# Kernel tuning notes

Hardware: AMD Instinct MI355X
Metric: run time of the kernel (lower is better)

The kernel has to match this reference:

```python
import jax, jax.numpy as jnp
import numpy as np

U, P, D, H, E = 512, 1024, 128, 256, 98304
N = U + P


def setup_inputs() -> dict:
    key = jax.random.key(0)
    ks = jax.random.split(key, 16)
    def nrm(k, shape, scale=0.05):
        return jax.random.normal(k, shape, jnp.float32) * scale
    z = lambda *s: jnp.zeros(s, jnp.float32)
    return {
        "user_ids": jnp.arange(U),
        "paper_ids": jnp.arange(P),
        "edge_index": jax.random.randint(ks[0], (2, E), 0, N),
        "user_paper_interactions": jax.random.uniform(ks[1], (U, P), jnp.float32),
        "user_emb": nrm(ks[2], (U, D), 1.0),   # nn.Embedding tables
        "paper_emb": nrm(ks[3], (P, D), 1.0),
        "W0": nrm(ks[4], (D, H)), "b0": z(H),   # GCNConv weights (stored [in,out])
        "W1": nrm(ks[5], (H, H)), "b1": z(H),
        "W2": nrm(ks[6], (H, H)), "b2": z(H),
        "Wu": nrm(ks[7], (H, D)), "bu": z(D),   # user_output Linear
        "Wp": nrm(ks[8], (H, D)), "bp": z(D),   # paper_output Linear
        "Wq1": nrm(ks[9], (2 * D, H)), "bq1": z(H),  # predictor Linear 1
        "Wq2": nrm(ks[10], (H, 1)), "bq2": z(1),      # predictor Linear 2
    }


def gcn_conv(x, src, dst, W, b):
    """PyG GCNConv: add self-loops, symmetric D^-1/2 (A+I) D^-1/2 normalization."""
    n = x.shape[0]
    loop = jnp.arange(n)
    s = jnp.concatenate([src, loop])
    d = jnp.concatenate([dst, loop])
    deg = jax.ops.segment_sum(jnp.ones(d.shape, x.dtype), d, num_segments=n)
    dis = jnp.where(deg > 0, jax.lax.rsqrt(jnp.maximum(deg, 1.0)), 0.0)
    norm = dis[s] * dis[d]                      # [E+n]
    h = x @ W                                   # [n, H]
    out = jax.ops.segment_sum(h[s] * norm[:, None], d, num_segments=n)
    return out + b


def reference(user_ids, paper_ids, edge_index, user_paper_interactions,
              user_emb, paper_emb, W0, b0, W1, b1, W2, b2,
              Wu, bu, Wp, bp, Wq1, bq1, Wq2, bq2):
    # embedding lookups + node feature matrix [U+P, D]
    x = jnp.concatenate([user_emb[user_ids], paper_emb[paper_ids]], axis=0)
    src, dst = edge_index[0], edge_index[1]
    for W, b in ((W0, b0), (W1, b1), (W2, b2)):
        x = jax.nn.relu(gcn_conv(x, src, dst, W, b))  # dropout is identity in eval
    nu = user_ids.shape[0]
    np_ = paper_ids.shape[0]
    user_final = x[:nu] @ Wu + bu               # [U, D]
    paper_final = x[nu:] @ Wp + bp              # [P, D]
    # broadcast outer-product concat -> [U, P, 2D]
    combined = jnp.concatenate([
        jnp.broadcast_to(user_final[:, None, :], (nu, np_, user_final.shape[-1])),
        jnp.broadcast_to(paper_final[None, :, :], (nu, np_, paper_final.shape[-1])),
    ], axis=-1)
    h = jax.nn.relu(combined @ Wq1 + bq1)       # [U, P, H]
    pred = jax.nn.sigmoid(h @ Wq2 + bq2)[..., 0]  # [U, P]
    return pred
```

## Files before the change

### kernel.cpp

```cpp
#include <hip/hip_runtime.h>
#include <math.h>

constexpr int Uc = 512;
constexpr int Pc = 1024;
constexpr int Dc = 128;
constexpr int Hc = 256;
constexpr int Ec = 98304;
constexpr int Nc = 1536;
constexpr int CAP = 192;

template <int K>
__device__ __forceinline__ void gemm_core16(const float* __restrict__ xr,
                                            const float* __restrict__ wc, int M,
                                            float& acc0, float& acc1) {
#pragma unroll 4
    for (int k = 0; k < K; k += 4) {
        float4 a = *(const float4*)(xr + k);
        float2 b0 = *(const float2*)(wc + (size_t)k * M);
        float2 b1 = *(const float2*)(wc + (size_t)(k + 1) * M);
        float2 b2 = *(const float2*)(wc + (size_t)(k + 2) * M);
        float2 b3 = *(const float2*)(wc + (size_t)(k + 3) * M);
        acc0 += a.x * b0.x; acc1 += a.x * b0.y;
        acc0 += a.y * b1.x; acc1 += a.y * b1.y;
        acc0 += a.z * b2.x; acc1 += a.z * b2.y;
        acc0 += a.w * b3.x; acc1 += a.w * b3.y;
    }
}

__global__ void k_front(const int* __restrict__ e_src, const int* __restrict__ e_dst,
                        int* __restrict__ cnt, int* __restrict__ colF,
                        const float* __restrict__ Wu, const float* __restrict__ Wp,
                        const float* __restrict__ Wq1, const float* __restrict__ bu,
                        const float* __restrict__ bp, const float* __restrict__ bq1,
                        float* __restrict__ Wup, float* __restrict__ Wpp,
                        float* __restrict__ bvu, float* __restrict__ bvp) {
    int t = threadIdx.x, b = blockIdx.x;
    if (b < 384) {
        int e = b * 256 + t;
        int d = e_dst[e];
        int pos = atomicAdd(&cnt[d], 1);
        if (pos < CAP) colF[d * CAP + pos] = e_src[e];
    } else if (b < 640) {
        int id = b - 384;
        int z = id >> 7, tile = id & 127;
        int tx = t & 15, ty = t >> 4;
        const float* X = z ? Wp : Wu;
        const float* W = Wq1 + (z ? (size_t)Dc * Hc : 0);
        float* Y = z ? Wpp : Wup;
        int row = (tile >> 3) * 16 + ty, col = (tile & 7) * 32 + tx * 2;
        float a0 = 0.f, a1 = 0.f;
        gemm_core16<Dc>(X + (size_t)row * Dc, W + col, Hc, a0, a1);
        *(float2*)&Y[(size_t)row * Hc + col] = make_float2(a0, a1);
    } else if (b == 640) {
        float s = bq1[t];
#pragma unroll 8
        for (int d = 0; d < Dc; d++) s += bu[d] * Wq1[d * Hc + t];
        bvu[t] = s;
    } else {
        float s = 0.f;
#pragma unroll 8
        for (int d = 0; d < Dc; d++) s += bp[d] * Wq1[(Dc + d) * Hc + t];
        bvp[t] = s;
    }
}

__global__ void k_l0(const int* __restrict__ uid, const int* __restrict__ pid,
                     const float* __restrict__ ue, const float* __restrict__ pe,
                     const float* __restrict__ W0, const float* __restrict__ b0,
                     const int* __restrict__ cnt, const int* __restrict__ colF,
                     float* __restrict__ out) {
    __shared__ const float* sptr[2][CAP];
    __shared__ float snrm[2][CAP];
    __shared__ __align__(16) float agg[2][Dc];
    int t = threadIdx.x, b = blockIdx.x;
    int i0 = b * 2, i1 = b * 2 + 1;
    int c0 = cnt[i0], c1 = cnt[i1];
    int deg0 = min(c0, CAP), deg1 = min(c1, CAP);
    float di0 = rsqrtf((float)(c0 + 1)), di1 = rsqrtf((float)(c1 + 1));
    if (t < deg0) {
        int s = colF[i0 * CAP + t];
        sptr[0][t] = (s < Uc) ? ue + (size_t)uid[s] * Dc : pe + (size_t)pid[s - Uc] * Dc;
        snrm[0][t] = rsqrtf((float)(cnt[s] + 1));
    }
    if (t < deg1) {
        int s = colF[i1 * CAP + t];
        sptr[1][t] = (s < Uc) ? ue + (size_t)uid[s] * Dc : pe + (size_t)pid[s - Uc] * Dc;
        snrm[1][t] = rsqrtf((float)(cnt[s] + 1));
    }
    __syncthreads();
    {
        int r = t >> 7, f = t & 127;
        int i = b * 2 + r;
        float di = r ? di1 : di0;
        int dg = r ? deg1 : deg0;
        const float* xi = (i < Uc) ? ue + (size_t)uid[i] * Dc : pe + (size_t)pid[i - Uc] * Dc;
        float acc = di * xi[f];
        int j = 0;
        for (; j + 4 <= dg; j += 4) {
            float v0 = snrm[r][j]     * sptr[r][j][f];
            float v1 = snrm[r][j + 1] * sptr[r][j + 1][f];
            float v2 = snrm[r][j + 2] * sptr[r][j + 2][f];
            float v3 = snrm[r][j + 3] * sptr[r][j + 3][f];
            acc += (v0 + v1) + (v2 + v3);
        }
        for (; j < dg; j++) acc += snrm[r][j] * sptr[r][j][f];
        agg[r][f] = di * acc;
    }
    __syncthreads();
    float acc0 = 0.f, acc1 = 0.f;
#pragma unroll 4
    for (int k = 0; k < Dc; k += 4) {
        float4 a0 = *(const float4*)&agg[0][k];
        float4 a1 = *(const float4*)&agg[1][k];
        float w0 = W0[(size_t)(k + 0) * Hc + t];
        float w1 = W0[(size_t)(k + 1) * Hc + t];
        float w2 = W0[(size_t)(k + 2) * Hc + t];
        float w3 = W0[(size_t)(k + 3) * Hc + t];
        acc0 += a0.x * w0 + a0.y * w1 + a0.z * w2 + a0.w * w3;
        acc1 += a1.x * w0 + a1.y * w1 + a1.z * w2 + a1.w * w3;
    }
    float bb = b0[t];
    out[(size_t)i0 * Hc + t] = fmaxf(acc0 + bb, 0.f);
    out[(size_t)i1 * Hc + t] = fmaxf(acc1 + bb, 0.f);
}

__global__ void k_lh(const float* __restrict__ X, const float* __restrict__ W,
                     const float* __restrict__ bias, const int* __restrict__ cnt,
                     const int* __restrict__ colF, float* __restrict__ out) {
    __shared__ int sidx[2][CAP];
    __shared__ float snrm[2][CAP];
    __shared__ __align__(16) float agg[2][Hc];
    int t = threadIdx.x, b = blockIdx.x;
    int i0 = b * 2, i1 = b * 2 + 1;
    int c0 = cnt[i0], c1 = cnt[i1];
    int deg0 = min(c0, CAP), deg1 = min(c1, CAP);
    float di0 = rsqrtf((float)(c0 + 1)), di1 = rsqrtf((float)(c1 + 1));
    if (t < deg0) {
        int s = colF[i0 * CAP + t];
        sidx[0][t] = s * Hc;
        snrm[0][t] = rsqrtf((float)(cnt[s] + 1));
    }
    if (t < deg1) {
        int s = colF[i1 * CAP + t];
        sidx[1][t] = s * Hc;
        snrm[1][t] = rsqrtf((float)(cnt[s] + 1));
    }
    __syncthreads();
    {
        float acc = di0 * X[(size_t)i0 * Hc + t];
        int j = 0;
        for (; j + 4 <= deg0; j += 4) {
            float v0 = snrm[0][j]     * X[sidx[0][j] + t];
            float v1 = snrm[0][j + 1] * X[sidx[0][j + 1] + t];
            float v2 = snrm[0][j + 2] * X[sidx[0][j + 2] + t];
            float v3 = snrm[0][j + 3] * X[sidx[0][j + 3] + t];
            acc += (v0 + v1) + (v2 + v3);
        }
        for (; j < deg0; j++) acc += snrm[0][j] * X[sidx[0][j] + t];
        agg[0][t] = di0 * acc;
    }
    {
        float acc = di1 * X[(size_t)i1 * Hc + t];
        int j = 0;
        for (; j + 4 <= deg1; j += 4) {
            float v0 = snrm[1][j]     * X[sidx[1][j] + t];
            float v1 = snrm[1][j + 1] * X[sidx[1][j + 1] + t];
            float v2 = snrm[1][j + 2] * X[sidx[1][j + 2] + t];
            float v3 = snrm[1][j + 3] * X[sidx[1][j + 3] + t];
            acc += (v0 + v1) + (v2 + v3);
        }
        for (; j < deg1; j++) acc += snrm[1][j] * X[sidx[1][j] + t];
        agg[1][t] = di1 * acc;
    }
    __syncthreads();
    float acc0 = 0.f, acc1 = 0.f;
#pragma unroll 4
    for (int k = 0; k < Hc; k += 4) {
        float4 a0 = *(const float4*)&agg[0][k];
        float4 a1 = *(const float4*)&agg[1][k];
        float w0 = W[(size_t)(k + 0) * Hc + t];
        float w1 = W[(size_t)(k + 1) * Hc + t];
        float w2 = W[(size_t)(k + 2) * Hc + t];
        float w3 = W[(size_t)(k + 3) * Hc + t];
        acc0 += a0.x * w0 + a0.y * w1 + a0.z * w2 + a0.w * w3;
        acc1 += a1.x * w0 + a1.y * w1 + a1.z * w2 + a1.w * w3;
    }
    float bb = bias[t];
    out[(size_t)i0 * Hc + t] = fmaxf(acc0 + bb, 0.f);
    out[(size_t)i1 * Hc + t] = fmaxf(acc1 + bb, 0.f);
}

__global__ void k_gemm_t(const float* __restrict__ xA, const float* __restrict__ Wup,
                         const float* __restrict__ Wpp, const float* __restrict__ bvu,
                         const float* __restrict__ bvp, float* __restrict__ AuT,
                         float* __restrict__ ApT) {
    int t = threadIdx.x, tx = t & 15, ty = t >> 4;
    int it = blockIdx.x;
    const float* X; const float* W; const float* bias; float* YT; int ldy; int id;
    if (it < 256) { X = xA;                   W = Wup; bias = bvu; YT = AuT; ldy = Uc; id = it; }
    else          { X = xA + (size_t)Uc * Hc; W = Wpp; bias = bvp; YT = ApT; ldy = Pc; id = it - 256; }
    int rloc = (id >> 3) * 16 + ty, col = (id & 7) * 32 + tx * 2;
    float a0 = 0.f, a1 = 0.f;
    gemm_core16<Hc>(X + (size_t)rloc * Hc, W + col, Hc, a0, a1);
    YT[(size_t)col * ldy + rloc]       = a0 + bias[col];
    YT[(size_t)(col + 1) * ldy + rloc] = a1 + bias[col + 1];
}

__global__ void k_pred(const float* __restrict__ AuT, const float* __restrict__ ApT,
                       const float* __restrict__ Wq2, const float* __restrict__ bq2,
                       float* __restrict__ out) {
    __shared__ float auS[Hc * 16];
    int t = threadIdx.x;
    int ub = blockIdx.x * 16, pb = blockIdx.y * 64;
#pragma unroll
    for (int i = t; i < Hc * 16; i += 256) {
        int k = i >> 4, u = i & 15;
        auS[i] = AuT[(size_t)k * Uc + ub + u];
    }
    __syncthreads();
    int uu = t >> 5;
    int pp = t & 31;
    const float* app = ApT + pb + pp * 2;
    const float* aup = auS + uu * 2;
    float acc[2][2] = {};
#pragma unroll 4
    for (int k = 0; k < Hc; k += 4) {
        float4 wv = *(const float4*)&Wq2[k];
        float2 a[4], p2[4];
#pragma unroll
        for (int j = 0; j < 4; j++) a[j] = *(const float2*)(aup + (k + j) * 16);
#pragma unroll
        for (int j = 0; j < 4; j++) p2[j] = *(const float2*)(app + (size_t)(k + j) * Pc);
        const float* w = (const float*)&wv;
#pragma unroll
        for (int j = 0; j < 4; j++) {
            float a0 = a[j].x, a1 = a[j].y;
            float p0 = p2[j].x, p1 = p2[j].y;
            acc[0][0] += fmaxf(a0 + p0, 0.f) * w[j];
            acc[0][1] += fmaxf(a0 + p1, 0.f) * w[j];
            acc[1][0] += fmaxf(a1 + p0, 0.f) * w[j];
            acc[1][1] += fmaxf(a1 + p1, 0.f) * w[j];
        }
    }
    float bq = bq2[0];
#pragma unroll
    for (int r = 0; r < 2; r++) {
        int u = ub + uu * 2 + r;
        float2 o;
        o.x = 1.f / (1.f + __expf(-(acc[r][0] + bq)));
        o.y = 1.f / (1.f + __expf(-(acc[r][1] + bq)));
        *(float2*)&out[(size_t)u * Pc + pb + pp * 2] = o;
    }
}


extern "C" void kernel_launch(void* const* d_in, const int* in_sizes, int n_in,
                              void* d_out, int out_size, void* d_ws, size_t ws_size,
                              hipStream_t stream) {
    const int*   uid = (const int*)d_in[0];
    const int*   pid = (const int*)d_in[1];
    const int*   ei  = (const int*)d_in[2];
    const float* ue  = (const float*)d_in[4];
    const float* pe  = (const float*)d_in[5];
    const float* W0  = (const float*)d_in[6];  const float* b0 = (const float*)d_in[7];
    const float* W1  = (const float*)d_in[8];  const float* b1 = (const float*)d_in[9];
    const float* W2  = (const float*)d_in[10]; const float* b2 = (const float*)d_in[11];
    const float* Wu  = (const float*)d_in[12]; const float* bu = (const float*)d_in[13];
    const float* Wp  = (const float*)d_in[14]; const float* bp = (const float*)d_in[15];
    const float* Wq1 = (const float*)d_in[16]; const float* bq1 = (const float*)d_in[17];
    const float* Wq2 = (const float*)d_in[18]; const float* bq2 = (const float*)d_in[19];

    const int* e_src = ei;
    const int* e_dst = ei + Ec;

    char* w = (char*)d_ws;
    auto alloc = [&](size_t bytes) { char* p = w; w += (bytes + 255) & ~size_t(255); return p; };
    int*   cnt  = (int*)alloc(Nc * 4);
    int*   colF = (int*)alloc((size_t)Nc * CAP * 4);
    float* xA   = (float*)alloc((size_t)Nc * Hc * 4);
    float* xB   = (float*)alloc((size_t)Nc * Hc * 4);
    float* Wup  = (float*)alloc((size_t)Hc * Hc * 4);
    float* Wpp  = (float*)alloc((size_t)Hc * Hc * 4);
    float* bvu  = (float*)alloc(Hc * 4);
    float* bvp  = (float*)alloc(Hc * 4);
    float* AuT  = (float*)alloc((size_t)Hc * Uc * 4);
    float* ApT  = (float*)alloc((size_t)Hc * Pc * 4);
    float* pred = (float*)d_out;

    hipMemsetAsync(cnt, 0, Nc * 4, stream);
    k_front<<<642, 256, 0, stream>>>(e_src, e_dst, cnt, colF, Wu, Wp, Wq1,
                                     bu, bp, bq1, Wup, Wpp, bvu, bvp);
    k_l0<<<Nc / 2, 256, 0, stream>>>(uid, pid, ue, pe, W0, b0, cnt, colF, xA);
    k_lh<<<Nc / 2, 256, 0, stream>>>(xA, W1, b1, cnt, colF, xB);
    k_lh<<<Nc / 2, 256, 0, stream>>>(xB, W2, b2, cnt, colF, xA);
    k_gemm_t<<<768, 256, 0, stream>>>(xA, Wup, Wpp, bvu, bvp, AuT, ApT);
    k_pred<<<dim3(Uc / 16, Pc / 64), 256, 0, stream>>>(AuT, ApT, Wq2, bq2, pred);
}
```

Before: 232.9 us.

## Process four nodes per block and fuse final GCN layer with output projection

```diff
diff --git a/kernel.cpp b/kernel.cpp
--- a/kernel.cpp
+++ b/kernel.cpp
@@ -69,32 +69,34 @@
                      const float* __restrict__ W0, const float* __restrict__ b0,
                      const int* __restrict__ cnt, const int* __restrict__ colF,
                      float* __restrict__ out) {
-    __shared__ const float* sptr[2][CAP];
-    __shared__ float snrm[2][CAP];
-    __shared__ __align__(16) float agg[2][Dc];
+    __shared__ const float* sptr[4][CAP];
+    __shared__ float snrm[4][CAP];
+    __shared__ __align__(16) float agg[4][Dc];
     int t = threadIdx.x, b = blockIdx.x;
-    int i0 = b * 2, i1 = b * 2 + 1;
-    int c0 = cnt[i0], c1 = cnt[i1];
-    int deg0 = min(c0, CAP), deg1 = min(c1, CAP);
-    float di0 = rsqrtf((float)(c0 + 1)), di1 = rsqrtf((float)(c1 + 1));
-    if (t < deg0) {
-        int s = colF[i0 * CAP + t];
-        sptr[0][t] = (s < Uc) ? ue + (size_t)uid[s] * Dc : pe + (size_t)pid[s - Uc] * Dc;
-        snrm[0][t] = rsqrtf((float)(cnt[s] + 1));
-    }
-    if (t < deg1) {
-        int s = colF[i1 * CAP + t];
-        sptr[1][t] = (s < Uc) ? ue + (size_t)uid[s] * Dc : pe + (size_t)pid[s - Uc] * Dc;
-        snrm[1][t] = rsqrtf((float)(cnt[s] + 1));
-    }
-    __syncthreads();
-    {
-        int r = t >> 7, f = t & 127;
-        int i = b * 2 + r;
-        float di = r ? di1 : di0;
-        int dg = r ? deg1 : deg0;
-        const float* xi = (i < Uc) ? ue + (size_t)uid[i] * Dc : pe + (size_t)pid[i - Uc] * Dc;
-        float acc = di * xi[f];
+    int ibase = b * 4;
+    int c[4]; float di[4];
+#pragma unroll
+    for (int r = 0; r < 4; r++) {
+        c[r] = cnt[ibase + r];
+        di[r] = rsqrtf((float)(c[r] + 1));
+        int deg = min(c[r], CAP);
+        if (t < deg) {
+            int s = colF[(ibase + r) * CAP + t];
+            sptr[r][t] = (s < Uc) ? ue + (size_t)uid[s] * Dc
+                                  : pe + (size_t)pid[s - Uc] * Dc;
+            snrm[r][t] = rsqrtf((float)(cnt[s] + 1));
+        }
+    }
+    __syncthreads();
+    int r2 = t >> 7, f = t & 127;
+#pragma unroll
+    for (int rr = 0; rr < 4; rr += 2) {
+        int r = rr + r2;
+        int i = ibase + r;
+        int dg = min(c[r], CAP);
+        const float* xi = (i < Uc) ? ue + (size_t)uid[i] * Dc
+                                   : pe + (size_t)pid[i - Uc] * Dc;
+        float acc = di[r] * xi[f];
         int j = 0;
         for (; j + 4 <= dg; j += 4) {
             float v0 = snrm[r][j]     * sptr[r][j][f];
@@ -104,106 +106,183 @@
             acc += (v0 + v1) + (v2 + v3);
         }
         for (; j < dg; j++) acc += snrm[r][j] * sptr[r][j][f];
-        agg[r][f] = di * acc;
-    }
-    __syncthreads();
-    float acc0 = 0.f, acc1 = 0.f;
-#pragma unroll 4
+        agg[r][f] = di[r] * acc;
+    }
+    __syncthreads();
+    float a0 = 0.f, a1 = 0.f, a2 = 0.f, a3 = 0.f;
+#pragma unroll 2
     for (int k = 0; k < Dc; k += 4) {
-        float4 a0 = *(const float4*)&agg[0][k];
-        float4 a1 = *(const float4*)&agg[1][k];
+        float4 g0 = *(const float4*)&agg[0][k];
+        float4 g1 = *(const float4*)&agg[1][k];
+        float4 g2 = *(const float4*)&agg[2][k];
+        float4 g3 = *(const float4*)&agg[3][k];
         float w0 = W0[(size_t)(k + 0) * Hc + t];
         float w1 = W0[(size_t)(k + 1) * Hc + t];
         float w2 = W0[(size_t)(k + 2) * Hc + t];
         float w3 = W0[(size_t)(k + 3) * Hc + t];
-        acc0 += a0.x * w0 + a0.y * w1 + a0.z * w2 + a0.w * w3;
-        acc1 += a1.x * w0 + a1.y * w1 + a1.z * w2 + a1.w * w3;
+        a0 += g0.x * w0 + g0.y * w1 + g0.z * w2 + g0.w * w3;
+        a1 += g1.x * w0 + g1.y * w1 + g1.z * w2 + g1.w * w3;
+        a2 += g2.x * w0 + g2.y * w1 + g2.z * w2 + g2.w * w3;
+        a3 += g3.x * w0 + g3.y * w1 + g3.z * w2 + g3.w * w3;
     }
     float bb = b0[t];
-    out[(size_t)i0 * Hc + t] = fmaxf(acc0 + bb, 0.f);
-    out[(size_t)i1 * Hc + t] = fmaxf(acc1 + bb, 0.f);
+    out[(size_t)(ibase + 0) * Hc + t] = fmaxf(a0 + bb, 0.f);
+    out[(size_t)(ibase + 1) * Hc + t] = fmaxf(a1 + bb, 0.f);
+    out[(size_t)(ibase + 2) * Hc + t] = fmaxf(a2 + bb, 0.f);
+    out[(size_t)(ibase + 3) * Hc + t] = fmaxf(a3 + bb, 0.f);
 }
 
 __global__ void k_lh(const float* __restrict__ X, const float* __restrict__ W,
                      const float* __restrict__ bias, const int* __restrict__ cnt,
                      const int* __restrict__ colF, float* __restrict__ out) {
-    __shared__ int sidx[2][CAP];
-    __shared__ float snrm[2][CAP];
-    __shared__ __align__(16) float agg[2][Hc];
+    __shared__ int sidx[4][CAP];
+    __shared__ float snrm[4][CAP];
+    __shared__ __align__(16) float agg[4][Hc];
     int t = threadIdx.x, b = blockIdx.x;
-    int i0 = b * 2, i1 = b * 2 + 1;
-    int c0 = cnt[i0], c1 = cnt[i1];
-    int deg0 = min(c0, CAP), deg1 = min(c1, CAP);
-    float di0 = rsqrtf((float)(c0 + 1)), di1 = rsqrtf((float)(c1 + 1));
-    if (t < deg0) {
-        int s = colF[i0 * CAP + t];
-        sidx[0][t] = s * Hc;
-        snrm[0][t] = rsqrtf((float)(cnt[s] + 1));
-    }
-    if (t < deg1) {
-        int s = colF[i1 * CAP + t];
-        sidx[1][t] = s * Hc;
-        snrm[1][t] = rsqrtf((float)(cnt[s] + 1));
-    }
-    __syncthreads();
-    {
-        float acc = di0 * X[(size_t)i0 * Hc + t];
+    int ibase = b * 4;
+    int c[4]; float di[4];
+#pragma unroll
+    for (int r = 0; r < 4; r++) {
+        c[r] = cnt[ibase + r];
+        di[r] = rsqrtf((float)(c[r] + 1));
+        int deg = min(c[r], CAP);
+        if (t < deg) {
+            int s = colF[(ibase + r) * CAP + t];
+            sidx[r][t] = s * Hc;
+            snrm[r][t] = rsqrtf((float)(cnt[s] + 1));
+        }
+    }
+    __syncthreads();
+#pragma unroll
+    for (int r = 0; r < 4; r++) {
+        int dg = min(c[r], CAP);
+        float acc = di[r] * X[(size_t)(ibase + r) * Hc + t];
         int j = 0;
-        for (; j + 4 <= deg0; j += 4) {
-            float v0 = snrm[0][j]     * X[sidx[0][j] + t];
-            float v1 = snrm[0][j + 1] * X[sidx[0][j + 1] + t];
-            float v2 = snrm[0][j + 2] * X[sidx[0][j + 2] + t];
-            float v3 = snrm[0][j + 3] * X[sidx[0][j + 3] + t];
+        for (; j + 4 <= dg; j += 4) {
+            float v0 = snrm[r][j]     * X[sidx[r][j] + t];
+            float v1 = snrm[r][j + 1] * X[sidx[r][j + 1] + t];
+            float v2 = snrm[r][j + 2] * X[sidx[r][j + 2] + t];
+            float v3 = snrm[r][j + 3] * X[sidx[r][j + 3] + t];
             acc += (v0 + v1) + (v2 + v3);
         }
-        for (; j < deg0; j++) acc += snrm[0][j] * X[sidx[0][j] + t];
-        agg[0][t] = di0 * acc;
-    }
-    {
-        float acc = di1 * X[(size_t)i1 * Hc + t];
-        int j = 0;
-        for (; j + 4 <= deg1; j += 4) {
-            float v0 = snrm[1][j]     * X[sidx[1][j] + t];
-            float v1 = snrm[1][j + 1] * X[sidx[1][j + 1] + t];
-            float v2 = snrm[1][j + 2] * X[sidx[1][j + 2] + t];
-            float v3 = snrm[1][j + 3] * X[sidx[1][j + 3] + t];
-            acc += (v0 + v1) + (v2 + v3);
-        }
-        for (; j < deg1; j++) acc += snrm[1][j] * X[sidx[1][j] + t];
-        agg[1][t] = di1 * acc;
-    }
-    __syncthreads();
-    float acc0 = 0.f, acc1 = 0.f;
-#pragma unroll 4
+        for (; j < dg; j++) acc += snrm[r][j] * X[sidx[r][j] + t];
+        agg[r][t] = di[r] * acc;
+    }
+    __syncthreads();
+    float a0 = 0.f, a1 = 0.f, a2 = 0.f, a3 = 0.f;
+#pragma unroll 2
     for (int k = 0; k < Hc; k += 4) {
-        float4 a0 = *(const float4*)&agg[0][k];
-        float4 a1 = *(const float4*)&agg[1][k];
+        float4 g0 = *(const float4*)&agg[0][k];
+        float4 g1 = *(const float4*)&agg[1][k];
+        float4 g2 = *(const float4*)&agg[2][k];
+        float4 g3 = *(const float4*)&agg[3][k];
         float w0 = W[(size_t)(k + 0) * Hc + t];
         float w1 = W[(size_t)(k + 1) * Hc + t];
         float w2 = W[(size_t)(k + 2) * Hc + t];
         float w3 = W[(size_t)(k + 3) * Hc + t];
-        acc0 += a0.x * w0 + a0.y * w1 + a0.z * w2 + a0.w * w3;
-        acc1 += a1.x * w0 + a1.y * w1 + a1.z * w2 + a1.w * w3;
+        a0 += g0.x * w0 + g0.y * w1 + g0.z * w2 + g0.w * w3;
+        a1 += g1.x * w0 + g1.y * w1 + g1.z * w2 + g1.w * w3;
+        a2 += g2.x * w0 + g2.y * w1 + g2.z * w2 + g2.w * w3;
+        a3 += g3.x * w0 + g3.y * w1 + g3.z * w2 + g3.w * w3;
     }
     float bb = bias[t];
-    out[(size_t)i0 * Hc + t] = fmaxf(acc0 + bb, 0.f);
-    out[(size_t)i1 * Hc + t] = fmaxf(acc1 + bb, 0.f);
-}
-
-__global__ void k_gemm_t(const float* __restrict__ xA, const float* __restrict__ Wup,
-                         const float* __restrict__ Wpp, const float* __restrict__ bvu,
-                         const float* __restrict__ bvp, float* __restrict__ AuT,
-                         float* __restrict__ ApT) {
-    int t = threadIdx.x, tx = t & 15, ty = t >> 4;
-    int it = blockIdx.x;
-    const float* X; const float* W; const float* bias; float* YT; int ldy; int id;
-    if (it < 256) { X = xA;                   W = Wup; bias = bvu; YT = AuT; ldy = Uc; id = it; }
-    else          { X = xA + (size_t)Uc * Hc; W = Wpp; bias = bvp; YT = ApT; ldy = Pc; id = it - 256; }
-    int rloc = (id >> 3) * 16 + ty, col = (id & 7) * 32 + tx * 2;
-    float a0 = 0.f, a1 = 0.f;
-    gemm_core16<Hc>(X + (size_t)rloc * Hc, W + col, Hc, a0, a1);
-    YT[(size_t)col * ldy + rloc]       = a0 + bias[col];
-    YT[(size_t)(col + 1) * ldy + rloc] = a1 + bias[col + 1];
+    out[(size_t)(ibase + 0) * Hc + t] = fmaxf(a0 + bb, 0.f);
+    out[(size_t)(ibase + 1) * Hc + t] = fmaxf(a1 + bb, 0.f);
+    out[(size_t)(ibase + 2) * Hc + t] = fmaxf(a2 + bb, 0.f);
+    out[(size_t)(ibase + 3) * Hc + t] = fmaxf(a3 + bb, 0.f);
+}
+
+__global__ void k_lht(const float* __restrict__ X, const float* __restrict__ W2,
+                      const float* __restrict__ b2, const int* __restrict__ cnt,
+                      const int* __restrict__ colF,
+                      const float* __restrict__ Wup, const float* __restrict__ Wpp,
+                      const float* __restrict__ bvu, const float* __restrict__ bvp,
+                      float* __restrict__ AuT, float* __restrict__ ApT) {
+    __shared__ int sidx[4][CAP];
+    __shared__ float snrm[4][CAP];
+    __shared__ __align__(16) float agg[4][Hc];
+    __shared__ __align__(16) float xloc[4][Hc];
+    int t = threadIdx.x, b = blockIdx.x;
+    int ibase = b * 4;
+    int c[4]; float di[4];
+#pragma unroll
+    for (int r = 0; r < 4; r++) {
+        c[r] = cnt[ibase + r];
+        di[r] = rsqrtf((float)(c[r] + 1));
+        int deg = min(c[r], CAP);
+        if (t < deg) {
+            int s = colF[(ibase + r) * CAP + t];
+            sidx[r][t] = s * Hc;
+            snrm[r][t] = rsqrtf((float)(cnt[s] + 1));
+        }
+    }
+    __syncthreads();
+#pragma unroll
+    for (int r = 0; r < 4; r++) {
+        int dg = min(c[r], CAP);
+        float acc = di[r] * X[(size_t)(ibase + r) * Hc + t];
+        int j = 0;
+        for (; j + 4 <= dg; j += 4) {
+            float v0 = snrm[r][j]     * X[sidx[r][j] + t];
+            float v1 = snrm[r][j + 1] * X[sidx[r][j + 1] + t];
+            float v2 = snrm[r][j + 2] * X[sidx[r][j + 2] + t];
+            float v3 = snrm[r][j + 3] * X[sidx[r][j + 3] + t];
+            acc += (v0 + v1) + (v2 + v3);
+        }
+        for (; j < dg; j++) acc += snrm[r][j] * X[sidx[r][j] + t];
+        agg[r][t] = di[r] * acc;
+    }
+    __syncthreads();
+    {
+        float a0 = 0.f, a1 = 0.f, a2 = 0.f, a3 = 0.f;
+#pragma unroll 2
+        for (int k = 0; k < Hc; k += 4) {
+            float4 g0 = *(const float4*)&agg[0][k];
+            float4 g1 = *(const float4*)&agg[1][k];
+            float4 g2 = *(const float4*)&agg[2][k];
+            float4 g3 = *(const float4*)&agg[3][k];
+            float w0 = W2[(size_t)(k + 0) * Hc + t];
+            float w1 = W2[(size_t)(k + 1) * Hc + t];
+            float w2 = W2[(size_t)(k + 2) * Hc + t];
+            float w3 = W2[(size_t)(k + 3) * Hc + t];
+            a0 += g0.x * w0 + g0.y * w1 + g0.z * w2 + g0.w * w3;
+            a1 += g1.x * w0 + g1.y * w1 + g1.z * w2 + g1.w * w3;
+            a2 += g2.x * w0 + g2.y * w1 + g2.z * w2 + g2.w * w3;
+            a3 += g3.x * w0 + g3.y * w1 + g3.z * w2 + g3.w * w3;
+        }
+        float bb = b2[t];
+        xloc[0][t] = fmaxf(a0 + bb, 0.f);
+        xloc[1][t] = fmaxf(a1 + bb, 0.f);
+        xloc[2][t] = fmaxf(a2 + bb, 0.f);
+        xloc[3][t] = fmaxf(a3 + bb, 0.f);
+    }
+    __syncthreads();
+    {
+        const float* Wsel = (b < 128) ? Wup : Wpp;
+        const float* bsel = (b < 128) ? bvu : bvp;
+        float* YT  = (b < 128) ? AuT : ApT;
+        int ldy    = (b < 128) ? Uc : Pc;
+        int rloc   = (b < 128) ? ibase : ibase - Uc;
+        float a0 = 0.f, a1 = 0.f, a2 = 0.f, a3 = 0.f;
+#pragma unroll 2
+        for (int k = 0; k < Hc; k += 4) {
+            float4 g0 = *(const float4*)&xloc[0][k];
+            float4 g1 = *(const float4*)&xloc[1][k];
+            float4 g2 = *(const float4*)&xloc[2][k];
+            float4 g3 = *(const float4*)&xloc[3][k];
+            float w0 = Wsel[(size_t)(k + 0) * Hc + t];
+            float w1 = Wsel[(size_t)(k + 1) * Hc + t];
+            float w2 = Wsel[(size_t)(k + 2) * Hc + t];
+            float w3 = Wsel[(size_t)(k + 3) * Hc + t];
+            a0 += g0.x * w0 + g0.y * w1 + g0.z * w2 + g0.w * w3;
+            a1 += g1.x * w0 + g1.y * w1 + g1.z * w2 + g1.w * w3;
+            a2 += g2.x * w0 + g2.y * w1 + g2.z * w2 + g2.w * w3;
+            a3 += g3.x * w0 + g3.y * w1 + g3.z * w2 + g3.w * w3;
+        }
+        float bb = bsel[t];
+        float4 o = make_float4(a0 + bb, a1 + bb, a2 + bb, a3 + bb);
+        *(float4*)&YT[(size_t)t * ldy + rloc] = o;
+    }
 }
 
 __global__ void k_pred(const float* __restrict__ AuT, const float* __restrict__ ApT,
@@ -290,9 +369,8 @@
     hipMemsetAsync(cnt, 0, Nc * 4, stream);
     k_front<<<642, 256, 0, stream>>>(e_src, e_dst, cnt, colF, Wu, Wp, Wq1,
                                      bu, bp, bq1, Wup, Wpp, bvu, bvp);
-    k_l0<<<Nc / 2, 256, 0, stream>>>(uid, pid, ue, pe, W0, b0, cnt, colF, xA);
-    k_lh<<<Nc / 2, 256, 0, stream>>>(xA, W1, b1, cnt, colF, xB);
-    k_lh<<<Nc / 2, 256, 0, stream>>>(xB, W2, b2, cnt, colF, xA);
-    k_gemm_t<<<768, 256, 0, stream>>>(xA, Wup, Wpp, bvu, bvp, AuT, ApT);
+    k_l0<<<Nc / 4, 256, 0, stream>>>(uid, pid, ue, pe, W0, b0, cnt, colF, xA);
+    k_lh<<<Nc / 4, 256, 0, stream>>>(xA, W1, b1, cnt, colF, xB);
+    k_lht<<<Nc / 4, 256, 0, stream>>>(xB, W2, b2, cnt, colF, Wup, Wpp, bvu, bvp, AuT, ApT);
     k_pred<<<dim3(Uc / 16, Pc / 64), 256, 0, stream>>>(AuT, ApT, Wq2, bq2, pred);
 }
```

After: 227.1 us. 2.5% less time.
